# Performance work log

Hardware: AMD Instinct MI355X
Metric: run time of the kernel (lower is better)

The kernel has to match this reference:

```python
import jax, jax.numpy as jnp
import numpy as np
import math

N = 4096      # nodes
E = 131072    # edges (avg degree 32)
C = 128       # input channels
RATIO = 0.5   # TopKPooling default ratio
DIMS = [(128, 256), (256, 512), (512, 512), (512, 256), (256, 128)]


def setup_inputs() -> dict:
    key = jax.random.key(0)
    ks = jax.random.split(key, 16)
    inp = {}
    inp['x'] = jax.random.normal(ks[0], (N, C), jnp.float32)
    inp['edge_index'] = jax.random.randint(ks[1], (2, E), 0, N, jnp.int32)
    for i, (fi, fo) in enumerate(DIMS):
        inp[f'w{i}'] = jax.random.normal(ks[2 + i], (fi, fo), jnp.float32) / np.sqrt(fi).astype(np.float32)
        inp[f'b{i}'] = jnp.zeros((fo,), jnp.float32)
    inp['p0'] = jax.random.normal(ks[10], (256,), jnp.float32)
    inp['p1'] = jax.random.normal(ks[11], (512,), jnp.float32)
    return inp


def _gcn(x, M, w, b):
    # GCNConv: add self loops (weight 1), symmetric D^-1/2 normalization with
    # deg computed over target (col) index, aggregate messages src->dst.
    # M[r, c] = weight of edge (src=r, dst=c); dense equivalent of sparse conv.
    n = M.shape[0]
    Mc = M + jnp.eye(n, dtype=M.dtype)
    deg = Mc.sum(axis=0)
    dis = jnp.where(deg > 0, jax.lax.rsqrt(deg), 0.0)
    A = dis[:, None] * Mc * dis[None, :]          # normalized (src, dst)
    return jax.nn.relu(A.T @ (x @ w) + b)          # out[dst] = sum_src A * xW


def _augment(M):
    # augment_adj: add self loops then spspmm(A, A) -> dense (M+I) @ (M+I)
    B = M + jnp.eye(M.shape[0], dtype=M.dtype)
    return B @ B


def _pool(x, M, p):
    # TopKPooling: score = tanh(x.p / ||p||), keep top ceil(ratio*n) nodes,
    # gate kept features by score, slice adjacency to kept nodes.
    s = jnp.tanh((x @ p) / jnp.linalg.norm(p))
    k = int(math.ceil(RATIO * x.shape[0]))
    vals, perm = jax.lax.top_k(s, k)
    return x[perm] * vals[:, None], M[perm][:, perm], perm


def reference(x, edge_index, w0, b0, w1, b1, w2, b2, w3, b3, w4, b4, p0, p1):
    # dense adjacency M[src, dst] from edge list with unit edge weights
    M = jnp.zeros((N, N), jnp.float32).at[edge_index[0], edge_index[1]].add(1.0)

    # down block 0
    x = _gcn(x, M, w0, b0)
    res0, M0 = x, M
    x, M, perm0 = _pool(x, _augment(M), p0)

    # down block 1
    x = _gcn(x, M, w1, b1)
    res1, M1 = x, M
    x, M, perm1 = _pool(x, _augment(M), p1)

    # bottleneck
    x = _gcn(x, M, w2, b2)

    # up block 1: scatter into zeros, sum residual
    up = jnp.zeros_like(res1).at[perm1].set(x)
    x = _gcn(res1 + up, M1, w3, b3)

    # up block 0
    up = jnp.zeros_like(res0).at[perm0].set(x)
    x = _gcn(res0 + up, M0, w4, b4)
    return x
```

## Files before the change

### kernel.cpp

```cpp
#include <hip/hip_runtime.h>

#define NN 4096
#define EE 131072
#define NP1 2048
#define NP2 1024

typedef __attribute__((ext_vector_type(8))) __bf16 bf16x8;
typedef __attribute__((ext_vector_type(4))) float f32x4;
typedef __attribute__((ext_vector_type(8))) unsigned short ushort8;

static __device__ inline unsigned short bfbits(__bf16 b) {
  union { __bf16 x; unsigned short u; } c; c.x = b; return c.u;
}
static __device__ inline void split2(float v, unsigned short& h, unsigned short& l) {
  __bf16 hb = (__bf16)v;
  float hf = (float)hb;
  __bf16 lb = (__bf16)(v - hf);
  h = bfbits(hb); l = bfbits(lb);
}

static __device__ inline size_t pchunk(int r, int k, int NT) {
  return ((size_t)(r >> 4) * NT + (k >> 5)) * 64 + (((k >> 3) & 3) << 4) + (r & 15);
}

static __device__ inline void tsplit_body(const float* in, unsigned short* oh, unsigned short* ol,
                                          int R, int C, int c) {
  int lane = c & 63, tile = c >> 6;
  int NT = R >> 5;
  int kt = tile % NT, jt = tile / NT;
  int j = jt * 16 + (lane & 15);
  int k = kt * 32 + (lane >> 4) * 8;
  ushort8 hv, lv;
#pragma unroll
  for (int e = 0; e < 8; ++e) {
    unsigned short he, le;
    split2(in[(size_t)(k + e) * C + j], he, le);
    hv[e] = he; lv[e] = le;
  }
  *(ushort8*)&oh[(size_t)c * 8] = hv;
  *(ushort8*)&ol[(size_t)c * 8] = lv;
}


__global__ __launch_bounds__(256) void prep_all(
    const int* __restrict__ esrc, const int* __restrict__ edst,
    int* __restrict__ cnt_src, int* __restrict__ cnt_dst,
    const float* w0, const float* w1, const float* w2, const float* w3, const float* w4,
    unsigned short* o0h, unsigned short* o0l, unsigned short* o1h, unsigned short* o1l,
    unsigned short* o2h, unsigned short* o2l, unsigned short* o3h, unsigned short* o3l,
    unsigned short* o4h, unsigned short* o4l,
    const float* p0, const float* p1, float* pnrm) {
  __shared__ float red[4];
  int b = blockIdx.x;
  int tid = threadIdx.x;
  if (b < EE / 256) {
    int e = b * 256 + tid;
    atomicAdd(&cnt_src[esrc[e]], 1);
    atomicAdd(&cnt_dst[edst[e]], 1);
  } else if (b < EE / 256 + 288) {
    int g = (b - EE / 256) * 256 + tid;
    if (g < 4096)        tsplit_body(w0, o0h, o0l, 128, 256, g);
    else if (g < 20480)  tsplit_body(w1, o1h, o1l, 256, 512, g - 4096);
    else if (g < 53248)  tsplit_body(w2, o2h, o2l, 512, 512, g - 20480);
    else if (g < 69632)  tsplit_body(w3, o3h, o3l, 512, 256, g - 53248);
    else                 tsplit_body(w4, o4h, o4l, 256, 128, g - 69632);
  } else {
    int which = b - (EE / 256 + 288);
    const float* p = which ? p1 : p0;
    int C = which ? 512 : 256;
    float acc = 0.f;
    for (int j = tid; j < C; j += 256) { float v = p[j]; acc += v * v; }
    for (int o = 32; o > 0; o >>= 1) acc += __shfl_down(acc, o);
    if ((tid & 63) == 0) red[tid >> 6] = acc;
    __syncthreads();
    if (tid == 0) pnrm[which] = sqrtf(red[0] + red[1] + red[2] + red[3]);
  }
}

__global__ __launch_bounds__(1024) void scan2(const int* __restrict__ cnt_dst,
                                              const int* __restrict__ cnt_src,
                                              int* __restrict__ csc_off, int* __restrict__ csr_off,
                                              float* __restrict__ dis0, int n) {
  __shared__ int tmp[4096];
  const int* in = blockIdx.x ? cnt_src : cnt_dst;
  int* out = blockIdx.x ? csr_off : csc_off;
  int tid = threadIdx.x;
  for (int i = tid; i < n; i += 1024) {
    int v = in[i];
    tmp[i] = v;
    if (blockIdx.x == 0) dis0[i] = rsqrtf((float)v + 1.0f);
  }
  __syncthreads();
  for (int off = 1; off < n; off <<= 1) {
    int v[4];
    int c = 0;
    for (int i = tid; i < n; i += 1024) { v[c++] = (i >= off) ? tmp[i - off] : 0; }
    __syncthreads();
    c = 0;
    for (int i = tid; i < n; i += 1024) { tmp[i] += v[c++]; }
    __syncthreads();
  }
  for (int i = tid; i < n; i += 1024) out[i + 1] = tmp[i];
  if (tid == 0) out[0] = 0;
}

__global__ void scatter_kernel(const int* __restrict__ src, const int* __restrict__ dst,
                               const int* __restrict__ csc_off, const int* __restrict__ csr_off,
                               int* __restrict__ fill_dst, int* __restrict__ fill_src,
                               int* __restrict__ csc_src, int* __restrict__ csr_dst, int E) {
  int e = blockIdx.x * blockDim.x + threadIdx.x;
  if (e < E) {
    int s = src[e], d = dst[e];
    int p = atomicAdd(&fill_dst[d], 1);
    csc_src[csc_off[d] + p] = s;
    int q = atomicAdd(&fill_src[s], 1);
    csr_dst[csr_off[s] + q] = d;
  }
}


__global__ void score_key(const float* __restrict__ X, const float* __restrict__ p,
                          const float* __restrict__ pn, float* __restrict__ s,
                          unsigned long long* __restrict__ keys, int C) {
  int i = blockIdx.x;
  int tid = threadIdx.x;
  float acc = 0.f;
  for (int j = tid; j < C; j += 256) acc += X[(size_t)i * C + j] * p[j];
  for (int o = 32; o > 0; o >>= 1) acc += __shfl_down(acc, o);
  __shared__ float red[4];
  if ((tid & 63) == 0) red[tid >> 6] = acc;
  __syncthreads();
  if (tid == 0) {
    float sv = tanhf((red[0] + red[1] + red[2] + red[3]) / pn[0]);
    s[i] = sv;
    unsigned u = __float_as_uint(sv);
    unsigned m = (u & 0x80000000u) ? ~u : (u | 0x80000000u);
    keys[i] = (((unsigned long long)(~m)) << 32) | (unsigned)i;
  }
}

__global__ __launch_bounds__(256) void rank_count(const unsigned long long* __restrict__ keys,
                                                  int* __restrict__ rank) {
  __shared__ unsigned long long kk[512];
  int tid = threadIdx.x;
  int cand = blockIdx.x * 256 + tid;
  int base = blockIdx.y * 512;
  kk[tid] = keys[base + tid];
  kk[tid + 256] = keys[base + tid + 256];
  __syncthreads();
  unsigned long long kc = keys[cand];
  int c = 0;
#pragma unroll 8
  for (int t = 0; t < 512; ++t) c += (kk[t] < kc) ? 1 : 0;
  atomicAdd(&rank[cand], c);
}

__global__ void rank_place(const float* __restrict__ s, const int* __restrict__ rank, int k, int n,
                           int* __restrict__ kept, int* __restrict__ perm, float* __restrict__ vals,
                           int* __restrict__ cntk) {
  int i = blockIdx.x * blockDim.x + threadIdx.x;
  if (i < n) {
    int r = rank[i];
    int isk = (r < k) ? 1 : 0;
    if (isk) { perm[r] = i; vals[r] = s[i]; kept[i] = r; }
    else kept[i] = -1;
    if (cntk) cntk[i] = isk;
  }
}

__global__ void pool_split_p(const float* __restrict__ X, const int* __restrict__ perm,
                             const float* __restrict__ vals, unsigned short* __restrict__ h,
                             unsigned short* __restrict__ l, int C) {
  int a = blockIdx.x;
  int r = perm[a];
  float v = vals[a];
  int NT = C >> 5;
  for (int j0 = threadIdx.x * 8; j0 < C; j0 += 64 * 8) {
    ushort8 hv, lv;
#pragma unroll
    for (int e = 0; e < 8; ++e) {
      unsigned short he, le;
      split2(X[(size_t)r * C + j0 + e] * v, he, le);
      hv[e] = he; lv[e] = le;
    }
    size_t c = pchunk(a, j0, NT);
    *(ushort8*)&h[c * 8] = hv;
    *(ushort8*)&l[c * 8] = lv;
  }
}

__global__ void pool_tsplit_p(const float* __restrict__ X, const int* __restrict__ perm,
                              const float* __restrict__ vals, const float* __restrict__ dis,
                              unsigned short* __restrict__ h, unsigned short* __restrict__ l) {
  int c = blockIdx.x * blockDim.x + threadIdx.x;
  int tile = c >> 6, lno = c & 63;
  int kt = tile & 63, jt = tile >> 6;
  int j = jt * 16 + (lno & 15);
  int k0 = kt * 32 + (lno >> 4) * 8;
  ushort8 hv, lv;
#pragma unroll
  for (int e = 0; e < 8; ++e) {
    int node = k0 + e;
    float sc = vals[node] * dis[node];
    float v = X[(size_t)perm[node] * 256 + j] * sc;
    unsigned short he, le;
    split2(v, he, le);
    hv[e] = he; lv[e] = le;
  }
  *(ushort8*)&h[(size_t)c * 8] = hv;
  *(ushort8*)&l[(size_t)c * 8] = lv;
}


__global__ __launch_bounds__(256) void augcnt(const int* __restrict__ csr_off,
                                              const int* __restrict__ csr_dst,
                                              const int* __restrict__ kept,
                                              const int* __restrict__ perm,
                                              unsigned short* __restrict__ rm,
                                              const int* __restrict__ esrc,
                                              const int* __restrict__ edst,
                                              int* __restrict__ cntk) {
  __shared__ float acc[NP1];
  int b = blockIdx.x;
  if (b < NP1) {
    int ki = b;
    int r = perm[ki];
    for (int t = threadIdx.x; t < NP1; t += 256) acc[t] = 0.f;
    __syncthreads();
    int s = csr_off[r], e = csr_off[r + 1];
    int nm = e - s;
    int wave = threadIdx.x >> 6, lane = threadIdx.x & 63;
    for (int m = wave; m <= nm; m += 4) {
      int k = (m < nm) ? csr_dst[s + m] : r;
      int s2 = csr_off[k], e2 = csr_off[k + 1];
      int n2 = e2 - s2;
      for (int t = lane; t <= n2; t += 64) {
        int j = (t < n2) ? csr_dst[s2 + t] : k;
        int kj = kept[j];
        if (kj >= 0) atomicAdd(&acc[kj], 1.0f);
      }
    }
    __syncthreads();
    if (threadIdx.x == 0) acc[ki] += 1.0f;
    __syncthreads();
    int tid = threadIdx.x;
    ushort8 hv;
#pragma unroll
    for (int e8 = 0; e8 < 8; ++e8) hv[e8] = bfbits((__bf16)acc[tid * 8 + e8]);
    size_t dst = (((size_t)(ki >> 4)) * 64 + (tid >> 2)) * 64 + (size_t)(tid & 3) * 16 + (ki & 15);
    *(ushort8*)&rm[dst * 8] = hv;
  } else {
    int e = (b - NP1) * 256 + threadIdx.x;
    if (kept[esrc[e]] >= 0) atomicAdd(&cntk[edst[e]], 1);
  }
}

__global__ __launch_bounds__(256) void degtp(const unsigned short* __restrict__ in,
                                             unsigned short* __restrict__ outp, int n,
                                             const int* __restrict__ csc_off,
                                             const int* __restrict__ csc_src,
                                             const int* __restrict__ cntk,
                                             const int* __restrict__ perm,
                                             float* __restrict__ dis) {
  __shared__ unsigned short t[64][72];
  int b = blockIdx.x;
  if (b < 1024) {
    int r0 = (b >> 5) * 64, c0 = (b & 31) * 64;
    int NT = n >> 5;
    for (int q = threadIdx.x; q < 512; q += 256) {
      int lt = q >> 6, l = q & 63;
      int rt = lt >> 1, kt2 = lt & 1;
      int r = rt * 16 + (l & 15), k = kt2 * 32 + (l >> 4) * 8;
      ushort8 v = *(const ushort8*)&in[pchunk(r0 + r, c0 + k, NT) * 8];
      *(ushort8*)&t[r][k] = v;
    }
    __syncthreads();
    for (int q = threadIdx.x; q < 512; q += 256) {
      int lt = q >> 6, l = q & 63;
      int jt = lt >> 1, kt2 = lt & 1;
      int j = jt * 16 + (l & 15), k = kt2 * 32 + (l >> 4) * 8;
      ushort8 v;
#pragma unroll
      for (int e = 0; e < 8; ++e) v[e] = t[k + e][j];
      *(ushort8*)&outp[pchunk(c0 + j, r0 + k, NT) * 8] = v;
    }
  } else {
    int bid = b - 1024;
    int wid = threadIdx.x >> 6, lane = threadIdx.x & 63;
    int c = bid * 4 + wid;
    int r = perm[c];
    int s = csc_off[r], e = csc_off[r + 1];
    int sum = 0;
    for (int t2 = s + lane; t2 < e; t2 += 64) sum += cntk[csc_src[t2]];
    for (int o = 32; o > 0; o >>= 1) sum += __shfl_down(sum, o);
    if (lane == 0) dis[c] = rsqrtf((float)(sum + cntk[r] + 1));
  }
}


__global__ void split_p(const float* __restrict__ in, unsigned short* __restrict__ h,
                        unsigned short* __restrict__ l, int K) {
  int c = blockIdx.x * blockDim.x + threadIdx.x;
  int lane = c & 63, tile = c >> 6;
  int NT = K >> 5;
  int kt = tile % NT, rt = tile / NT;
  int r = rt * 16 + (lane & 15);
  int k = kt * 32 + (lane >> 4) * 8;
  const float* p = in + (size_t)r * K + k;
  ushort8 hv, lv;
#pragma unroll
  for (int e = 0; e < 8; ++e) {
    unsigned short he, le;
    split2(p[e], he, le);
    hv[e] = he; lv[e] = le;
  }
  *(ushort8*)&h[(size_t)c * 8] = hv;
  *(ushort8*)&l[(size_t)c * 8] = lv;
}

__global__ void gather2_p(const unsigned short* __restrict__ in0, const unsigned short* __restrict__ in1,
                          const int* __restrict__ perm,
                          unsigned short* __restrict__ out0, unsigned short* __restrict__ out1, int NT) {
  const unsigned short* in = blockIdx.y ? in1 : in0;
  unsigned short* outp = blockIdx.y ? out1 : out0;
  int c = blockIdx.x * blockDim.x + threadIdx.x;
  int lane = c & 63, tile = c >> 6;
  int kt = tile % NT, at = tile / NT;
  int a = at * 16 + (lane & 15);
  int sub = lane >> 4;
  int p = perm[a];
  size_t sc = ((size_t)(p >> 4) * NT + kt) * 64 + sub * 16 + (p & 15);
  *(ushort8*)&outp[(size_t)c * 8] = *(const ushort8*)&in[sc * 8];
}

__global__ void unpool_split_p(const float* __restrict__ res, const float* __restrict__ up,
                               const int* __restrict__ kept, unsigned short* __restrict__ h,
                               unsigned short* __restrict__ l, int C) {
  int c = blockIdx.x * blockDim.x + threadIdx.x;
  int lane = c & 63, tile = c >> 6;
  int NT = C >> 5;
  int kt = tile % NT, rt = tile / NT;
  int r = rt * 16 + (lane & 15);
  int j0 = kt * 32 + (lane >> 4) * 8;
  int kv = kept[r];
  ushort8 hv, lv;
#pragma unroll
  for (int e = 0; e < 8; ++e) {
    float v = res[(size_t)r * C + j0 + e];
    if (kv >= 0) v += up[(size_t)kv * C + j0 + e];
    unsigned short he, le;
    split2(v, he, le);
    hv[e] = he; lv[e] = le;
  }
  *(ushort8*)&h[(size_t)c * 8] = hv;
  *(ushort8*)&l[(size_t)c * 8] = lv;
}


template <int C>
__global__ __launch_bounds__(256) void spmm_pre(const float* __restrict__ X,
                                                const int* __restrict__ off,
                                                const int* __restrict__ srcs,
                                                const float* __restrict__ dis,
                                                float* __restrict__ out) {
  constexpr int VEC = C / 64;
  int w = threadIdx.x >> 6, lane = threadIdx.x & 63;
  int c = blockIdx.x * 4 + w;
  int j = lane * VEC;
  float dc = dis[c];
  float acc[VEC];
  const float* p = X + (size_t)c * C + j;
#pragma unroll
  for (int u = 0; u < VEC; ++u) acc[u] = dc * p[u];
  int s = off[c], e = off[c + 1];
  for (int t = s; t < e; ++t) {
    int sr = srcs[t];
    float ds = dis[sr];
    const float* q = X + (size_t)sr * C + j;
#pragma unroll
    for (int u = 0; u < VEC; ++u) acc[u] += ds * q[u];
  }
  float* o = out + (size_t)c * C + j;
#pragma unroll
  for (int u = 0; u < VEC; ++u) o[u] = dc * acc[u];
}

template <int C>
__global__ __launch_bounds__(256) void spmm_gather_v(const float* __restrict__ Y,
                                                     const int* __restrict__ off,
                                                     const int* __restrict__ srcs,
                                                     const float* __restrict__ dis,
                                                     const float* __restrict__ bias,
                                                     float* __restrict__ out) {
  constexpr int VEC = C / 64;
  int w = threadIdx.x >> 6, lane = threadIdx.x & 63;
  int c = blockIdx.x * 4 + w;
  int j = lane * VEC;
  float acc[VEC];
  const float* p = Y + (size_t)c * C + j;
#pragma unroll
  for (int u = 0; u < VEC; ++u) acc[u] = p[u];
  int s = off[c], e = off[c + 1];
  for (int t = s; t < e; ++t) {
    const float* q = Y + (size_t)srcs[t] * C + j;
#pragma unroll
    for (int u = 0; u < VEC; ++u) acc[u] += q[u];
  }
  float d = dis[c];
  float* o = out + (size_t)c * C + j;
#pragma unroll
  for (int u = 0; u < VEC; ++u) o[u] = fmaxf(d * acc[u] + bias[j + u], 0.0f);
}


template <int S, int RSQ>
__global__ void ep3(const float* __restrict__ p, const float* __restrict__ rs,
                    const float* __restrict__ bias, float* __restrict__ outp, int M, int N) {
  int idx = blockIdx.x * blockDim.x + threadIdx.x;
  int j4 = (idx * 4) % N, i = (idx * 4) / N;
  float4 a = {0.f, 0.f, 0.f, 0.f};
#pragma unroll
  for (int s = 0; s < S; ++s) {
    float4 b = *(const float4*)(p + ((size_t)s * M + i) * N + j4);
    a.x += b.x; a.y += b.y; a.z += b.z; a.w += b.w;
  }
  float r = rs[i];
  if (RSQ) r = rsqrtf(r);
  float4 o;
  o.x = fmaxf(r * a.x + bias[j4 + 0], 0.f);
  o.y = fmaxf(r * a.y + bias[j4 + 1], 0.f);
  o.z = fmaxf(r * a.z + bias[j4 + 2], 0.f);
  o.w = fmaxf(r * a.w + bias[j4 + 3], 0.f);
  *(float4*)(outp + (size_t)i * N + j4) = o;
}

template <int S>
__global__ void ep_zsplit(const float* __restrict__ p, unsigned short* __restrict__ h,
                          unsigned short* __restrict__ l, int M, int N) {
  int t = blockIdx.x * blockDim.x + threadIdx.x;
  int tile = t >> 6, w = t & 63;
  int NT = N >> 5;
  int rt = tile / NT, kt = tile % NT;
  int r = rt * 16 + (w & 15);
  int k = kt * 32 + (w >> 4) * 8;
  const float* p0 = p + (size_t)r * N + k;
  ushort8 hv, lv;
#pragma unroll
  for (int e = 0; e < 8; ++e) {
    float v = p0[e];
#pragma unroll
    for (int s = 1; s < S; ++s) v += p0[(size_t)s * M * N + e];
    unsigned short he, le;
    split2(v, he, le);
    hv[e] = he; lv[e] = le;
  }
  *(ushort8*)&h[(size_t)t * 8] = hv;
  *(ushort8*)&l[(size_t)t * 8] = lv;
}

template <int S>
__global__ void ep_aug_cs2(const float* __restrict__ p, unsigned short* __restrict__ th,
                           unsigned short* __restrict__ tl, float* __restrict__ deg, int n) {
  int c = blockIdx.x * 256 + threadIdx.x;
  int r0 = blockIdx.y * 64;
  int NT = n >> 5;
  float cs = 0.f;
  for (int g = 0; g < 8; ++g) {
    float vbuf[8];
#pragma unroll
    for (int e = 0; e < 8; ++e) {
      int r = r0 + g * 8 + e;
      float v = 0.f;
#pragma unroll
      for (int s = 0; s < S; ++s) v += p[((size_t)s * n + r) * n + c];
      if (r == c) v += 1.0f;
      vbuf[e] = v;
      cs += v;
    }
    ushort8 hv, lv;
#pragma unroll
    for (int e = 0; e < 8; ++e) {
      unsigned short he, le;
      split2(vbuf[e], he, le);
      hv[e] = he; lv[e] = le;
    }
    size_t ch = pchunk(c, r0 + g * 8, NT);
    *(ushort8*)&th[ch * 8] = hv;
    *(ushort8*)&tl[ch * 8] = lv;
  }
  atomicAdd(&deg[c], cs);
}

template <int EPI, int AL, int BL, int KK, int S, int RSQ>
__global__ __launch_bounds__(256) void gemm16(
    const unsigned short* __restrict__ Ah, const unsigned short* __restrict__ Al,
    const unsigned short* __restrict__ Bh, const unsigned short* __restrict__ Bl,
    int M, int N, const float* __restrict__ rs, const float* __restrict__ bias,
    float* __restrict__ C, unsigned short* __restrict__ Th, unsigned short* __restrict__ Tl) {
  static_assert(KK % 32 == 0, "K");
  constexpr int KSTEPS = KK / 32;
  const int NT = (KK * S) >> 5;
  const int gx = gridDim.x;
  int id = blockIdx.y * gx + blockIdx.x;
  int cpx = (gx * gridDim.y) >> 3;
  int sid = (id & 7) * cpx + (id >> 3);
  const int bx = sid % gx, by = sid / gx;
  const int z = (S > 1) ? blockIdx.z : 0;
  const int wid = threadIdx.x >> 6, lane = threadIdx.x & 63;
  const int i0 = by * 64 + (wid >> 1) * 32;
  const int j0 = bx * 64 + (wid & 1) * 32;
  const int lr = lane & 15, lk = lane >> 4;
  size_t aoff[2], boff[2];
#pragma unroll
  for (int t = 0; t < 2; ++t) {
    aoff[t] = ((size_t)((i0 >> 4) + t) * NT + z * (KK >> 5)) * 512 + lane * 8;
    boff[t] = ((size_t)((j0 >> 4) + t) * NT + z * (KK >> 5)) * 512 + lane * 8;
  }
  const f32x4 zf = {0.f, 0.f, 0.f, 0.f};
  f32x4 acc[2][2];
  acc[0][0] = zf; acc[0][1] = zf; acc[1][0] = zf; acc[1][1] = zf;

  bf16x8 ahf[4][2], bhf[4][2], alf[4][2], blf[4][2];
  auto loadk = [&](int kk, int b) {
    size_t o = (size_t)kk * 512;
    ahf[b][0] = *(const bf16x8*)(Ah + aoff[0] + o);
    ahf[b][1] = *(const bf16x8*)(Ah + aoff[1] + o);
    bhf[b][0] = *(const bf16x8*)(Bh + boff[0] + o);
    bhf[b][1] = *(const bf16x8*)(Bh + boff[1] + o);
    if constexpr (AL) {
      alf[b][0] = *(const bf16x8*)(Al + aoff[0] + o);
      alf[b][1] = *(const bf16x8*)(Al + aoff[1] + o);
    }
    if constexpr (BL) {
      blf[b][0] = *(const bf16x8*)(Bl + boff[0] + o);
      blf[b][1] = *(const bf16x8*)(Bl + boff[1] + o);
    }
  };
  auto domm = [&](int b) {
#pragma unroll
    for (int am = 0; am < 2; ++am)
#pragma unroll
      for (int bn = 0; bn < 2; ++bn) {
        acc[am][bn] = __builtin_amdgcn_mfma_f32_16x16x32_bf16(ahf[b][am], bhf[b][bn], acc[am][bn], 0, 0, 0);
        if constexpr (BL)
          acc[am][bn] = __builtin_amdgcn_mfma_f32_16x16x32_bf16(ahf[b][am], blf[b][bn], acc[am][bn], 0, 0, 0);
        if constexpr (AL)
          acc[am][bn] = __builtin_amdgcn_mfma_f32_16x16x32_bf16(alf[b][am], bhf[b][bn], acc[am][bn], 0, 0, 0);
      }
  };

  loadk(0, 0);
  if constexpr (KSTEPS > 1) loadk(1, 1);
  if constexpr (KSTEPS > 2) loadk(2, 2);
#pragma unroll
  for (int kk = 0; kk < KSTEPS; ++kk) {
    const int cur = kk & 3;
    if (kk + 3 < KSTEPS) loadk(kk + 3, (cur + 3) & 3);
    domm(cur);
  }

#pragma unroll
  for (int am = 0; am < 2; ++am)
#pragma unroll
    for (int bn = 0; bn < 2; ++bn) {
      int ib = i0 + 16 * am + lk * 4;
      int j = j0 + 16 * bn + lr;
      f32x4 a = acc[am][bn];
      if constexpr (S > 1) {
#pragma unroll
        for (int r = 0; r < 4; ++r) C[((size_t)z * M + ib + r) * N + j] = a[r];
      } else if constexpr (EPI == 0) {
#pragma unroll
        for (int r = 0; r < 4; ++r) C[(size_t)(ib + r) * N + j] = a[r];
      } else if constexpr (EPI == 1) {
#pragma unroll
        for (int r = 0; r < 4; ++r) {
          float rsv = rs[ib + r];
          if (RSQ) rsv = rsqrtf(rsv);
          C[(size_t)(ib + r) * N + j] = rsv * a[r];
        }
      } else if constexpr (EPI == 2) {
        unsigned long long hp = 0, lp = 0;
#pragma unroll
        for (int r = 0; r < 4; ++r) {
          float rsv = rs[ib + r];
          if (RSQ) rsv = rsqrtf(rsv);
          unsigned short hv, lv;
          split2(rsv * a[r], hv, lv);
          hp |= ((unsigned long long)hv) << (16 * r);
          lp |= ((unsigned long long)lv) << (16 * r);
        }
        size_t c = pchunk(j, ib, M >> 5);
        *(unsigned long long*)&Th[c * 8 + (ib & 7)] = hp;
        *(unsigned long long*)&Tl[c * 8 + (ib & 7)] = lp;
      } else if constexpr (EPI == 3) {
#pragma unroll
        for (int r = 0; r < 4; ++r) {
          float rsv = rs[ib + r];
          if (RSQ) rsv = rsqrtf(rsv);
          C[(size_t)(ib + r) * N + j] = fmaxf(rsv * a[r] + bias[j], 0.0f);
        }
      } else {
#pragma unroll
        for (int r = 0; r < 4; ++r)
          C[(size_t)(ib + r) * N + j] = fmaxf(a[r] + bias[j], 0.0f);
      }
    }
}

template <int AL, int BL, int KK, int S>
__global__ __launch_bounds__(256) void gemm64(
    const unsigned short* __restrict__ Ah, const unsigned short* __restrict__ Al,
    const unsigned short* __restrict__ Bh, const unsigned short* __restrict__ Bl,
    int M, int N, float* __restrict__ C) {
  static_assert(KK % 32 == 0, "K");
  constexpr int KSTEPS = KK / 32;
  const int NT = (KK * S) >> 5;
  const int gx = gridDim.x;
  int id = blockIdx.y * gx + blockIdx.x;
  int cpx = (gx * gridDim.y) >> 3;
  int sid = (id & 7) * cpx + (id >> 3);
  const int bx = sid % gx, by = sid / gx;
  const int z = blockIdx.z;
  const int wid = threadIdx.x >> 6, lane = threadIdx.x & 63;
  const int i0 = by * 128 + (wid >> 1) * 64;
  const int j0 = bx * 128 + (wid & 1) * 64;
  const int lr = lane & 15, lk = lane >> 4;
  size_t aoff[4], boff[4];
#pragma unroll
  for (int t = 0; t < 4; ++t) {
    aoff[t] = ((size_t)((i0 >> 4) + t) * NT + z * (KK >> 5)) * 512 + lane * 8;
    boff[t] = ((size_t)((j0 >> 4) + t) * NT + z * (KK >> 5)) * 512 + lane * 8;
  }
  const f32x4 zf = {0.f, 0.f, 0.f, 0.f};
  f32x4 acc[4][4];
#pragma unroll
  for (int a = 0; a < 4; ++a)
#pragma unroll
    for (int b = 0; b < 4; ++b) acc[a][b] = zf;

  bf16x8 ahf[2][4], bhf[2][4], alf[2][4], blf[2][4];
  auto loadk = [&](int kk, int b) {
    size_t o = (size_t)kk * 512;
#pragma unroll
    for (int t = 0; t < 4; ++t) {
      ahf[b][t] = *(const bf16x8*)(Ah + aoff[t] + o);
      bhf[b][t] = *(const bf16x8*)(Bh + boff[t] + o);
      if constexpr (AL) alf[b][t] = *(const bf16x8*)(Al + aoff[t] + o);
      if constexpr (BL) blf[b][t] = *(const bf16x8*)(Bl + boff[t] + o);
    }
  };
  auto domm = [&](int b) {
#pragma unroll
    for (int am = 0; am < 4; ++am)
#pragma unroll
      for (int bn = 0; bn < 4; ++bn) {
        acc[am][bn] = __builtin_amdgcn_mfma_f32_16x16x32_bf16(ahf[b][am], bhf[b][bn], acc[am][bn], 0, 0, 0);
        if constexpr (BL)
          acc[am][bn] = __builtin_amdgcn_mfma_f32_16x16x32_bf16(ahf[b][am], blf[b][bn], acc[am][bn], 0, 0, 0);
        if constexpr (AL)
          acc[am][bn] = __builtin_amdgcn_mfma_f32_16x16x32_bf16(alf[b][am], bhf[b][bn], acc[am][bn], 0, 0, 0);
      }
  };

  loadk(0, 0);
#pragma unroll
  for (int kk = 0; kk < KSTEPS; ++kk) {
    const int cur = kk & 1;
    if (kk + 1 < KSTEPS) loadk(kk + 1, cur ^ 1);
    domm(cur);
  }

#pragma unroll
  for (int am = 0; am < 4; ++am)
#pragma unroll
    for (int bn = 0; bn < 4; ++bn) {
      int ib = i0 + 16 * am + lk * 4;
      int j = j0 + 16 * bn + lr;
      f32x4 a = acc[am][bn];
#pragma unroll
      for (int r = 0; r < 4; ++r) C[((size_t)z * M + ib + r) * N + j] = a[r];
    }
}


extern "C" void kernel_launch(void* const* d_in, const int* in_sizes, int n_in,
                              void* d_out, int out_size, void* d_ws, size_t ws_size,
                              hipStream_t stream) {
  (void)in_sizes; (void)n_in; (void)out_size; (void)ws_size;
  const float* x  = (const float*)d_in[0];
  const int* ei   = (const int*)d_in[1];
  const int* esrc = ei;
  const int* edst = ei + EE;
  const float* w0 = (const float*)d_in[2];
  const float* b0 = (const float*)d_in[3];
  const float* w1 = (const float*)d_in[4];
  const float* b1 = (const float*)d_in[5];
  const float* w2 = (const float*)d_in[6];
  const float* b2 = (const float*)d_in[7];
  const float* w3 = (const float*)d_in[8];
  const float* b3 = (const float*)d_in[9];
  const float* w4 = (const float*)d_in[10];
  const float* b4 = (const float*)d_in[11];
  const float* p0 = (const float*)d_in[12];
  const float* p1 = (const float*)d_in[13];
  float* out = (float*)d_out;

  char* ws = (char*)d_ws;
  size_t off = 0;
  auto alloc = [&](size_t b) { void* p = ws + off; off += (b + 255) & ~(size_t)255; return p; };

  int* csc_off = (int*)alloc(4 * (NN + 1));
  int* csr_off = (int*)alloc(4 * (NN + 1));
  int* csc_src = (int*)alloc(4 * EE);
  int* csr_dst = (int*)alloc(4 * EE);

  size_t zero_bytes = 4 * NN * 4 + 4 * NP2 + 4 * NN + 4 * NP1;
  int* cnts    = (int*)alloc(zero_bytes);
  int* cnt_dst = cnts;
  int* cnt_src = cnts + NN;
  int* fill_dst = cnts + 2 * NN;
  int* fill_src = cnts + 3 * NN;
  float* deg2 = (float*)(cnts + 4 * NN);
  int* rank0 = (int*)(deg2 + NP2);
  int* rank1 = rank0 + NN;

  int* cntk  = (int*)alloc(4 * NN);
  int* kept0 = (int*)alloc(4 * NN);
  int* perm0 = (int*)alloc(4 * NP1);
  int* kept1 = (int*)alloc(4 * NP1);
  int* perm1 = (int*)alloc(4 * NP2);
  float* dis0 = (float*)alloc(4 * NN);
  float* dis1 = (float*)alloc(4 * NP1);
  float* pnrm = (float*)alloc(8);
  float* s0   = (float*)alloc(4 * NN);
  float* vals0 = (float*)alloc(4 * NP1);
  float* s1   = (float*)alloc(4 * NP1);
  float* vals1 = (float*)alloc(4 * NP2);
  unsigned long long* keys0 = (unsigned long long*)alloc(8 * NN);
  unsigned long long* keys1 = (unsigned long long*)alloc(8 * NP1);

  const size_t MB = 1024 * 1024;
  char* regB1 = (char*)alloc(16 * MB);
  unsigned short* Gh2 = (unsigned short*)regB1;
  unsigned short* Hh2 = (unsigned short*)(regB1 + 4 * MB);
  unsigned short* B2th = (unsigned short*)(regB1 + 4 * MB);
  unsigned short* B2tl = (unsigned short*)(regB1 + 6 * MB);
  float* pscr = (float*)alloc(16 * MB);

  unsigned short* B1rm = (unsigned short*)alloc(8 * MB);
  unsigned short* B1t  = (unsigned short*)alloc(8 * MB);
  float* res0 = (float*)alloc(4 * MB);
  float* res1 = (float*)alloc(4 * MB);
  float* yreg = (float*)alloc(4 * MB);
  float* Gspmm = yreg;
  float* outreg = (float*)alloc(2 * MB);
  float* out2 = outreg, *out3 = outreg;
  char* ytreg = (char*)alloc(4 * MB);
  unsigned short* Y2th = (unsigned short*)ytreg;
  unsigned short* Y2tl = (unsigned short*)(ytreg + 1 * MB);
  unsigned short* Y3th = (unsigned short*)ytreg;
  unsigned short* Y3tl = (unsigned short*)(ytreg + 1 * MB);
  char* xsreg = (char*)alloc(4 * MB);
  unsigned short* x3h = (unsigned short*)xsreg;
  unsigned short* x3l = (unsigned short*)(xsreg + 2 * MB);
  unsigned short* x4h = (unsigned short*)xsreg;
  unsigned short* x4l = (unsigned short*)(xsreg + 2 * MB);
  unsigned short* xh = (unsigned short*)alloc(1 * MB);
  unsigned short* xl = (unsigned short*)alloc(1 * MB);
  char* xsm = (char*)alloc(2 * MB);
  unsigned short* x1th = (unsigned short*)xsm;
  unsigned short* x1tl = (unsigned short*)(xsm + 1 * MB);
  unsigned short* Zh = (unsigned short*)xsm;
  unsigned short* Zl = (unsigned short*)(xsm + 1 * MB);
  unsigned short* x2h = (unsigned short*)xsm;
  unsigned short* x2l = (unsigned short*)(xsm + 1 * MB);
  unsigned short* Wt0h = (unsigned short*)alloc(256 * 128 * 2);
  unsigned short* Wt0l = (unsigned short*)alloc(256 * 128 * 2);
  unsigned short* Wt1h = (unsigned short*)alloc(512 * 256 * 2);
  unsigned short* Wt1l = (unsigned short*)alloc(512 * 256 * 2);
  unsigned short* Wt2h = (unsigned short*)alloc(512 * 512 * 2);
  unsigned short* Wt2l = (unsigned short*)alloc(512 * 512 * 2);
  unsigned short* Wt3h = (unsigned short*)alloc(256 * 512 * 2);
  unsigned short* Wt3l = (unsigned short*)alloc(256 * 512 * 2);
  unsigned short* Wt4h = (unsigned short*)alloc(128 * 256 * 2);
  unsigned short* Wt4l = (unsigned short*)alloc(128 * 256 * 2);

  hipMemsetAsync(cnts, 0, zero_bytes, stream);

  prep_all<<<EE / 256 + 288 + 2, 256, 0, stream>>>(
      esrc, edst, cnt_src, cnt_dst, w0, w1, w2, w3, w4,
      Wt0h, Wt0l, Wt1h, Wt1l, Wt2h, Wt2l, Wt3h, Wt3l, Wt4h, Wt4l, p0, p1, pnrm);
  scan2<<<2, 1024, 0, stream>>>(cnt_dst, cnt_src, csc_off, csr_off, dis0, NN);
  scatter_kernel<<<EE / 256, 256, 0, stream>>>(esrc, edst, csc_off, csr_off,
                                               fill_dst, fill_src, csc_src, csr_dst, EE);

  spmm_pre<128><<<NN / 4, 256, 0, stream>>>(x, csc_off, csc_src, dis0, Gspmm);
  split_p<<<(NN * 128 / 8) / 256, 256, 0, stream>>>(Gspmm, xh, xl, 128);
  gemm16<4, 1, 1, 128, 1, 0><<<dim3(4, 64), 256, 0, stream>>>(xh, xl, Wt0h, Wt0l,
                                                              NN, 256, nullptr, b0, res0, nullptr, nullptr);

  score_key<<<NN, 256, 0, stream>>>(res0, p0, pnrm + 0, s0, keys0, 256);
  rank_count<<<dim3(NN / 256, NN / 512), 256, 0, stream>>>(keys0, rank0);
  rank_place<<<NN / 256, 256, 0, stream>>>(s0, rank0, NP1, NN, kept0, perm0, vals0, cntk);

  augcnt<<<NP1 + EE / 256, 256, 0, stream>>>(csr_off, csr_dst, kept0, perm0, B1rm,
                                             esrc, edst, cntk);
  degtp<<<1024 + NP1 / 4, 256, 0, stream>>>(B1rm, B1t, NP1, csc_off, csc_src, cntk, perm0, dis1);

  pool_tsplit_p<<<(NP1 * 256 / 8) / 256, 256, 0, stream>>>(res0, perm0, vals0, dis1, x1th, x1tl);
  gemm16<0, 0, 1, 1024, 2, 0><<<dim3(4, 32, 2), 256, 0, stream>>>(B1t, nullptr, x1th, x1tl,
                                                                  NP1, 256, nullptr, nullptr, pscr, nullptr, nullptr);
  ep_zsplit<2><<<(NP1 * 256 / 8) / 256, 256, 0, stream>>>(pscr, Zh, Zl, NP1, 256);
  gemm16<3, 1, 1, 256, 1, 0><<<dim3(8, 32), 256, 0, stream>>>(Zh, Zl, Wt1h, Wt1l,
                                                              NP1, 512, dis1, b1, res1, nullptr, nullptr);

  score_key<<<NP1, 256, 0, stream>>>(res1, p1, pnrm + 1, s1, keys1, 512);
  rank_count<<<dim3(NP1 / 256, NP1 / 512), 256, 0, stream>>>(keys1, rank1);
  rank_place<<<NP1 / 256, 256, 0, stream>>>(s1, rank1, NP2, NP1, kept1, perm1, vals1, nullptr);
  pool_split_p<<<NP2, 64, 0, stream>>>(res1, perm1, vals1, x2h, x2l, 512);

  gather2_p<<<dim3((NP2 * NP1 / 8) / 256, 2), 256, 0, stream>>>(B1rm, B1t, perm1, Gh2, Hh2, NP1 >> 5);
  gemm64<0, 0, 512, 4><<<dim3(8, 8, 4), 256, 0, stream>>>(Gh2, nullptr, Hh2, nullptr,
                                                          NP2, NP2, pscr);
  ep_aug_cs2<4><<<dim3(NP2 / 256, NP2 / 64), 256, 0, stream>>>(pscr, B2th, B2tl, deg2, NP2);

  gemm16<2, 1, 1, 512, 1, 1><<<dim3(8, 16), 256, 0, stream>>>(x2h, x2l, Wt2h, Wt2l,
                                                              NP2, 512, deg2, nullptr, nullptr, Y2th, Y2tl);
  gemm16<0, 1, 1, 512, 2, 0><<<dim3(8, 16, 2), 256, 0, stream>>>(B2th, B2tl, Y2th, Y2tl,
                                                                 NP2, 512, nullptr, nullptr, pscr, nullptr, nullptr);
  ep3<2, 1><<<(NP2 * 512) / 1024, 256, 0, stream>>>(pscr, deg2, b2, out2, NP2, 512);

  unpool_split_p<<<(NP1 * 512 / 8) / 256, 256, 0, stream>>>(res1, out2, kept1, x3h, x3l, 512);
  gemm16<2, 1, 1, 512, 1, 0><<<dim3(4, 32), 256, 0, stream>>>(x3h, x3l, Wt3h, Wt3l,
                                                              NP1, 256, dis1, nullptr, nullptr, Y3th, Y3tl);
  gemm64<0, 1, 256, 8><<<dim3(2, 16, 8), 256, 0, stream>>>(B1t, nullptr, Y3th, Y3tl,
                                                           NP1, 256, pscr);
  ep3<8, 0><<<(NP1 * 256) / 1024, 256, 0, stream>>>(pscr, dis1, b3, out3, NP1, 256);

  unpool_split_p<<<(NN * 256 / 8) / 256, 256, 0, stream>>>(res0, out3, kept0, x4h, x4l, 256);
  gemm16<1, 1, 1, 256, 1, 0><<<dim3(2, 64), 256, 0, stream>>>(x4h, x4l, Wt4h, Wt4l,
                                                              NN, 128, dis0, nullptr, yreg, nullptr, nullptr);
  spmm_gather_v<128><<<NN / 4, 256, 0, stream>>>(yreg, csc_off, csc_src, dis0, b4, out);
}
```

Baseline: 312.1 us.

## Fuse split, gather and epilogue kernels to cut launches and intermediate buffers

```diff
diff --git a/kernel.cpp b/kernel.cpp
--- a/kernel.cpp
+++ b/kernel.cpp
@@ -168,27 +168,6 @@
   }
 }
 
-__global__ void pool_split_p(const float* __restrict__ X, const int* __restrict__ perm,
-                             const float* __restrict__ vals, unsigned short* __restrict__ h,
-                             unsigned short* __restrict__ l, int C) {
-  int a = blockIdx.x;
-  int r = perm[a];
-  float v = vals[a];
-  int NT = C >> 5;
-  for (int j0 = threadIdx.x * 8; j0 < C; j0 += 64 * 8) {
-    ushort8 hv, lv;
-#pragma unroll
-    for (int e = 0; e < 8; ++e) {
-      unsigned short he, le;
-      split2(X[(size_t)r * C + j0 + e] * v, he, le);
-      hv[e] = he; lv[e] = le;
-    }
-    size_t c = pchunk(a, j0, NT);
-    *(ushort8*)&h[c * 8] = hv;
-    *(ushort8*)&l[c * 8] = lv;
-  }
-}
-
 __global__ void pool_tsplit_p(const float* __restrict__ X, const int* __restrict__ perm,
                               const float* __restrict__ vals, const float* __restrict__ dis,
                               unsigned short* __restrict__ h, unsigned short* __restrict__ l) {
@@ -209,6 +188,47 @@
   }
   *(ushort8*)&h[(size_t)c * 8] = hv;
   *(ushort8*)&l[(size_t)c * 8] = lv;
+}
+
+__global__ __launch_bounds__(256) void pool1_misc(
+    const float* __restrict__ res1, const int* __restrict__ perm1, const float* __restrict__ vals1,
+    unsigned short* __restrict__ x2h, unsigned short* __restrict__ x2l,
+    const unsigned short* __restrict__ B1rm, const unsigned short* __restrict__ B1t,
+    unsigned short* __restrict__ Gh2, unsigned short* __restrict__ Hh2) {
+  int b = blockIdx.x;
+  int tid = threadIdx.x;
+  if (b < 256) {
+    int c = b * 256 + tid;
+    int lane = c & 63, tile = c >> 6;
+    int kt = tile & 15, rt = tile >> 4;
+    int r = rt * 16 + (lane & 15);
+    int k0 = kt * 32 + (lane >> 4) * 8;
+    float v = vals1[r];
+    const float* src = res1 + (size_t)perm1[r] * 512 + k0;
+    ushort8 hv, lv;
+#pragma unroll
+    for (int e = 0; e < 8; ++e) {
+      unsigned short he, le;
+      split2(src[e] * v, he, le);
+      hv[e] = he; lv[e] = le;
+    }
+    *(ushort8*)&x2h[(size_t)c * 8] = hv;
+    *(ushort8*)&x2l[(size_t)c * 8] = lv;
+  } else {
+    int idx = b - 256;
+    int mat = idx >> 10;
+    int c = (idx & 1023) * 256 + tid;
+    const unsigned short* in = mat ? B1t : B1rm;
+    unsigned short* outp = mat ? Hh2 : Gh2;
+    const int NT = NP1 >> 5;
+    int lane = c & 63, tile = c >> 6;
+    int kt = tile % NT, at = tile / NT;
+    int a = at * 16 + (lane & 15);
+    int sub = lane >> 4;
+    int p = perm1[a];
+    size_t sc = ((size_t)(p >> 4) * NT + kt) * 64 + sub * 16 + (p & 15);
+    *(ushort8*)&outp[(size_t)c * 8] = *(const ushort8*)&in[sc * 8];
+  }
 }
 
 
@@ -298,71 +318,14 @@
 }
 
 
-__global__ void split_p(const float* __restrict__ in, unsigned short* __restrict__ h,
-                        unsigned short* __restrict__ l, int K) {
-  int c = blockIdx.x * blockDim.x + threadIdx.x;
-  int lane = c & 63, tile = c >> 6;
-  int NT = K >> 5;
-  int kt = tile % NT, rt = tile / NT;
-  int r = rt * 16 + (lane & 15);
-  int k = kt * 32 + (lane >> 4) * 8;
-  const float* p = in + (size_t)r * K + k;
-  ushort8 hv, lv;
-#pragma unroll
-  for (int e = 0; e < 8; ++e) {
-    unsigned short he, le;
-    split2(p[e], he, le);
-    hv[e] = he; lv[e] = le;
-  }
-  *(ushort8*)&h[(size_t)c * 8] = hv;
-  *(ushort8*)&l[(size_t)c * 8] = lv;
-}
-
-__global__ void gather2_p(const unsigned short* __restrict__ in0, const unsigned short* __restrict__ in1,
-                          const int* __restrict__ perm,
-                          unsigned short* __restrict__ out0, unsigned short* __restrict__ out1, int NT) {
-  const unsigned short* in = blockIdx.y ? in1 : in0;
-  unsigned short* outp = blockIdx.y ? out1 : out0;
-  int c = blockIdx.x * blockDim.x + threadIdx.x;
-  int lane = c & 63, tile = c >> 6;
-  int kt = tile % NT, at = tile / NT;
-  int a = at * 16 + (lane & 15);
-  int sub = lane >> 4;
-  int p = perm[a];
-  size_t sc = ((size_t)(p >> 4) * NT + kt) * 64 + sub * 16 + (p & 15);
-  *(ushort8*)&outp[(size_t)c * 8] = *(const ushort8*)&in[sc * 8];
-}
-
-__global__ void unpool_split_p(const float* __restrict__ res, const float* __restrict__ up,
-                               const int* __restrict__ kept, unsigned short* __restrict__ h,
-                               unsigned short* __restrict__ l, int C) {
-  int c = blockIdx.x * blockDim.x + threadIdx.x;
-  int lane = c & 63, tile = c >> 6;
-  int NT = C >> 5;
-  int kt = tile % NT, rt = tile / NT;
-  int r = rt * 16 + (lane & 15);
-  int j0 = kt * 32 + (lane >> 4) * 8;
-  int kv = kept[r];
-  ushort8 hv, lv;
-#pragma unroll
-  for (int e = 0; e < 8; ++e) {
-    float v = res[(size_t)r * C + j0 + e];
-    if (kv >= 0) v += up[(size_t)kv * C + j0 + e];
-    unsigned short he, le;
-    split2(v, he, le);
-    hv[e] = he; lv[e] = le;
-  }
-  *(ushort8*)&h[(size_t)c * 8] = hv;
-  *(ushort8*)&l[(size_t)c * 8] = lv;
-}
-
-
 template <int C>
-__global__ __launch_bounds__(256) void spmm_pre(const float* __restrict__ X,
-                                                const int* __restrict__ off,
-                                                const int* __restrict__ srcs,
-                                                const float* __restrict__ dis,
-                                                float* __restrict__ out) {
+__global__ __launch_bounds__(256) void spmm_presplit(const float* __restrict__ X,
+                                                     const int* __restrict__ off,
+                                                     const int* __restrict__ srcs,
+                                                     const float* __restrict__ dis,
+                                                     unsigned short* __restrict__ h,
+                                                     unsigned short* __restrict__ l) {
+  __shared__ float buf[4][C];
   constexpr int VEC = C / 64;
   int w = threadIdx.x >> 6, lane = threadIdx.x & 63;
   int c = blockIdx.x * 4 + w;
@@ -380,9 +343,23 @@
 #pragma unroll
     for (int u = 0; u < VEC; ++u) acc[u] += ds * q[u];
   }
-  float* o = out + (size_t)c * C + j;
-#pragma unroll
-  for (int u = 0; u < VEC; ++u) o[u] = dc * acc[u];
+#pragma unroll
+  for (int u = 0; u < VEC; ++u) buf[w][j + u] = dc * acc[u];
+  __syncthreads();
+  constexpr int NC = C / 8;
+  if (lane < NC) {
+    const float* src = &buf[w][lane * 8];
+    ushort8 hv, lv;
+#pragma unroll
+    for (int e2 = 0; e2 < 8; ++e2) {
+      unsigned short he, le;
+      split2(src[e2], he, le);
+      hv[e2] = he; lv[e2] = le;
+    }
+    size_t ch = pchunk(c, lane * 8, C >> 5);
+    *(ushort8*)&h[ch * 8] = hv;
+    *(ushort8*)&l[ch * 8] = lv;
+  }
 }
 
 template <int C>
@@ -413,27 +390,6 @@
 }
 
 
-template <int S, int RSQ>
-__global__ void ep3(const float* __restrict__ p, const float* __restrict__ rs,
-                    const float* __restrict__ bias, float* __restrict__ outp, int M, int N) {
-  int idx = blockIdx.x * blockDim.x + threadIdx.x;
-  int j4 = (idx * 4) % N, i = (idx * 4) / N;
-  float4 a = {0.f, 0.f, 0.f, 0.f};
-#pragma unroll
-  for (int s = 0; s < S; ++s) {
-    float4 b = *(const float4*)(p + ((size_t)s * M + i) * N + j4);
-    a.x += b.x; a.y += b.y; a.z += b.z; a.w += b.w;
-  }
-  float r = rs[i];
-  if (RSQ) r = rsqrtf(r);
-  float4 o;
-  o.x = fmaxf(r * a.x + bias[j4 + 0], 0.f);
-  o.y = fmaxf(r * a.y + bias[j4 + 1], 0.f);
-  o.z = fmaxf(r * a.z + bias[j4 + 2], 0.f);
-  o.w = fmaxf(r * a.w + bias[j4 + 3], 0.f);
-  *(float4*)(outp + (size_t)i * N + j4) = o;
-}
-
 template <int S>
 __global__ void ep_zsplit(const float* __restrict__ p, unsigned short* __restrict__ h,
                           unsigned short* __restrict__ l, int M, int N) {
@@ -456,6 +412,39 @@
   }
   *(ushort8*)&h[(size_t)t * 8] = hv;
   *(ushort8*)&l[(size_t)t * 8] = lv;
+}
+
+template <int S, int RSQ>
+__global__ void unpool_ep_split(const float* __restrict__ res, const float* __restrict__ pscr,
+                                const int* __restrict__ kept, const float* __restrict__ rs,
+                                const float* __restrict__ bias,
+                                unsigned short* __restrict__ h, unsigned short* __restrict__ l,
+                                int M, int C) {
+  int c = blockIdx.x * blockDim.x + threadIdx.x;
+  int lane = c & 63, tile = c >> 6;
+  int NT = C >> 5;
+  int kt = tile % NT, rt = tile / NT;
+  int r = rt * 16 + (lane & 15);
+  int j0 = kt * 32 + (lane >> 4) * 8;
+  int kv = kept[r];
+  float rsv = 0.f;
+  if (kv >= 0) { rsv = rs[kv]; if (RSQ) rsv = rsqrtf(rsv); }
+  ushort8 hv, lv;
+#pragma unroll
+  for (int e = 0; e < 8; ++e) {
+    float v = res[(size_t)r * C + j0 + e];
+    if (kv >= 0) {
+      float a = 0.f;
+#pragma unroll
+      for (int s = 0; s < S; ++s) a += pscr[((size_t)s * M + kv) * C + j0 + e];
+      v += fmaxf(rsv * a + bias[j0 + e], 0.0f);
+    }
+    unsigned short he, le;
+    split2(v, he, le);
+    hv[e] = he; lv[e] = le;
+  }
+  *(ushort8*)&h[(size_t)c * 8] = hv;
+  *(ushort8*)&l[(size_t)c * 8] = lv;
 }
 
 template <int S>
@@ -753,9 +742,6 @@
   float* res0 = (float*)alloc(4 * MB);
   float* res1 = (float*)alloc(4 * MB);
   float* yreg = (float*)alloc(4 * MB);
-  float* Gspmm = yreg;
-  float* outreg = (float*)alloc(2 * MB);
-  float* out2 = outreg, *out3 = outreg;
   char* ytreg = (char*)alloc(4 * MB);
   unsigned short* Y2th = (unsigned short*)ytreg;
   unsigned short* Y2tl = (unsigned short*)(ytreg + 1 * MB);
@@ -795,8 +781,7 @@
   scatter_kernel<<<EE / 256, 256, 0, stream>>>(esrc, edst, csc_off, csr_off,
                                                fill_dst, fill_src, csc_src, csr_dst, EE);
 
-  spmm_pre<128><<<NN / 4, 256, 0, stream>>>(x, csc_off, csc_src, dis0, Gspmm);
-  split_p<<<(NN * 128 / 8) / 256, 256, 0, stream>>>(Gspmm, xh, xl, 128);
+  spmm_presplit<128><<<NN / 4, 256, 0, stream>>>(x, csc_off, csc_src, dis0, xh, xl);
   gemm16<4, 1, 1, 128, 1, 0><<<dim3(4, 64), 256, 0, stream>>>(xh, xl, Wt0h, Wt0l,
                                                               NN, 256, nullptr, b0, res0, nullptr, nullptr);
 
@@ -818,9 +803,10 @@
   score_key<<<NP1, 256, 0, stream>>>(res1, p1, pnrm + 1, s1, keys1, 512);
   rank_count<<<dim3(NP1 / 256, NP1 / 512), 256, 0, stream>>>(keys1, rank1);
   rank_place<<<NP1 / 256, 256, 0, stream>>>(s1, rank1, NP2, NP1, kept1, perm1, vals1, nullptr);
-  pool_split_p<<<NP2, 64, 0, stream>>>(res1, perm1, vals1, x2h, x2l, 512);
-
-  gather2_p<<<dim3((NP2 * NP1 / 8) / 256, 2), 256, 0, stream>>>(B1rm, B1t, perm1, Gh2, Hh2, NP1 >> 5);
+
+  pool1_misc<<<256 + 2048, 256, 0, stream>>>(res1, perm1, vals1, x2h, x2l,
+                                             B1rm, B1t, Gh2, Hh2);
+
   gemm64<0, 0, 512, 4><<<dim3(8, 8, 4), 256, 0, stream>>>(Gh2, nullptr, Hh2, nullptr,
                                                           NP2, NP2, pscr);
   ep_aug_cs2<4><<<dim3(NP2 / 256, NP2 / 64), 256, 0, stream>>>(pscr, B2th, B2tl, deg2, NP2);
@@ -829,16 +815,16 @@
                                                               NP2, 512, deg2, nullptr, nullptr, Y2th, Y2tl);
   gemm16<0, 1, 1, 512, 2, 0><<<dim3(8, 16, 2), 256, 0, stream>>>(B2th, B2tl, Y2th, Y2tl,
                                                                  NP2, 512, nullptr, nullptr, pscr, nullptr, nullptr);
-  ep3<2, 1><<<(NP2 * 512) / 1024, 256, 0, stream>>>(pscr, deg2, b2, out2, NP2, 512);
-
-  unpool_split_p<<<(NP1 * 512 / 8) / 256, 256, 0, stream>>>(res1, out2, kept1, x3h, x3l, 512);
+
+  unpool_ep_split<2, 1><<<(NP1 * 512 / 8) / 256, 256, 0, stream>>>(res1, pscr, kept1, deg2, b2,
+                                                                   x3h, x3l, NP2, 512);
   gemm16<2, 1, 1, 512, 1, 0><<<dim3(4, 32), 256, 0, stream>>>(x3h, x3l, Wt3h, Wt3l,
                                                               NP1, 256, dis1, nullptr, nullptr, Y3th, Y3tl);
   gemm64<0, 1, 256, 8><<<dim3(2, 16, 8), 256, 0, stream>>>(B1t, nullptr, Y3th, Y3tl,
                                                            NP1, 256, pscr);
-  ep3<8, 0><<<(NP1 * 256) / 1024, 256, 0, stream>>>(pscr, dis1, b3, out3, NP1, 256);
-
-  unpool_split_p<<<(NN * 256 / 8) / 256, 256, 0, stream>>>(res0, out3, kept0, x4h, x4l, 256);
+
+  unpool_ep_split<8, 0><<<(NN * 256 / 8) / 256, 256, 0, stream>>>(res0, pscr, kept0, dis1, b3,
+                                                                  x4h, x4l, NP1, 256);
   gemm16<1, 1, 1, 256, 1, 0><<<dim3(2, 64), 256, 0, stream>>>(x4h, x4l, Wt4h, Wt4l,
                                                               NN, 128, dis0, nullptr, yreg, nullptr, nullptr);
   spmm_gather_v<128><<<NN / 4, 256, 0, stream>>>(yreg, csc_off, csc_src, dis0, b4, out);
```

Result: no change. 312.5 us (+0.1%).
